# Kernel optimization log

Hardware: AMD Instinct MI355X
Metric: run time of the kernel (lower is better)

## Reference

```python
import jax, jax.numpy as jnp
from jax import lax
import numpy as np

# ---- SLAYER SRM-alpha neuron / simulation constants (net_params) ----
THETA = 10.0      # spiking threshold
TAU_SR = 1.0      # PSP (synaptic response) time constant
TAU_REF = 1.0     # refractory time constant
TS = 1.0          # simulation timestep
POOL_GAIN = 1.1 * THETA  # SLAYER pool layer uses fixed weights = 1.1*theta (sum pool)

# SRM alpha kernel eps[n] = (n*Ts/tau) * exp(1 - n*Ts/tau) = c * n * d^n with
#   d = exp(-Ts/tau), c = e*Ts/tau.  Causal convolution with this kernel obeys
# a 2nd-order linear recurrence, so we implement psp as a lax.scan over time
# (the "recursive exponential temporal filter" the original does via temporal conv).

def psp(x):
    """Alpha-kernel temporal filter along last (time) axis."""
    d = float(np.exp(-TS / TAU_SR))
    c = float(np.e * TS / TAU_SR)
    xt = jnp.moveaxis(x, -1, 0)  # (T, ...)
    z = jnp.zeros_like(xt[0])
    def step(carry, u):
        p, q = carry
        q = d * (q + p)       # q[t] = sum_{n>=1} n d^n x[t-n]
        p = d * p + u         # p[t] = sum_{n>=0} d^n x[t-n]
        return (p, q), c * q
    _, y = lax.scan(step, (z, z), xt)
    return jnp.moveaxis(y, 0, -1)


def spike(u):
    """SLAYER spike generation: threshold the membrane potential at theta and
    subtract a refractory alpha kernel (-2*theta * alpha(tauRef)) from the
    future potential after each spike. Sequential scan over time."""
    d = float(np.exp(-TS / TAU_REF))
    c_r = float(-2.0 * THETA * np.e * TS / TAU_REF)
    ut = jnp.moveaxis(u, -1, 0)  # (T, ...)
    z = jnp.zeros_like(ut[0])
    def step(carry, u_t):
        p, q = carry
        q = d * (q + p)                       # refractory filter state
        s = (u_t + c_r * q >= THETA).astype(u_t.dtype)
        p = d * p + s                         # spikes feed the refractory filter
        return (p, q), s
    _, s = lax.scan(step, (z, z), ut)
    return jnp.moveaxis(s, 0, -1) / TS


def pool(x, k):
    """SLAYER pool: conv with fixed weight 1.1*theta (sum pool scaled)."""
    B, C, H, W, T = x.shape
    xr = x.reshape(B, C, H // k, k, W // k, k, T)
    return POOL_GAIN * xr.sum(axis=(3, 5))


def conv2d_t(x, W, pad):
    """Per-timestep 2D conv (SLAYER conv has time-kernel 1, no bias)."""
    B, C, H, Wd, T = x.shape
    xf = jnp.moveaxis(x, -1, 1).reshape(B * T, C, H, Wd)
    y = lax.conv_general_dilated(xf, W, (1, 1), [(pad, pad), (pad, pad)],
                                 dimension_numbers=('NCHW', 'OIHW', 'NCHW'))
    O, Ho, Wo = y.shape[1], y.shape[2], y.shape[3]
    return jnp.moveaxis(y.reshape(B, T, O, Ho, Wo), 1, -1)


def setup_inputs() -> dict:
    key = jax.random.key(0)
    ks = jax.random.split(key, 5)
    B, T = 8, 300
    s_in = jax.random.bernoulli(ks[0], 0.1, (B, 2, 128, 128, T)).astype(jnp.float32)
    # weightScale 10/50/... only affects init magnitude; choose scales that
    # produce non-degenerate spiking activity.
    W1 = jax.random.normal(ks[1], (16, 2, 5, 5), jnp.float32) * 0.5
    W2 = jax.random.normal(ks[2], (32, 16, 3, 3), jnp.float32) * 0.2
    Wf1 = jax.random.normal(ks[3], (512, 32, 8, 8), jnp.float32) * 0.05
    Wf2 = jax.random.normal(ks[4], (11, 512), jnp.float32) * 0.2
    return {"s_in": s_in, "W1": W1, "W2": W2, "Wf1": Wf1, "Wf2": Wf2}


def reference(s_in, W1, W2, Wf1, Wf2):
    s = spike(psp(pool(s_in, 4)))                 # SP0: (B,2,32,32,T)
    s = spike(psp(conv2d_t(s, W1, 2)))            # SC1: (B,16,32,32,T)
    s = spike(psp(pool(s, 2)))                    # SP1: (B,16,16,16,T)
    # SDC dropout p=0.0 -> identity
    s = spike(psp(conv2d_t(s, W2, 1)))            # SC2: (B,32,16,16,T)
    s = spike(psp(pool(s, 2)))                    # SP2: (B,32,8,8,T)
    # SDF dropout p=0.0 -> identity
    s = spike(psp(jnp.einsum('bchwt,ochw->bot', s, Wf1)))  # SF1: (B,512,T)
    s = spike(psp(jnp.einsum('bct,oc->bot', s, Wf2)))      # SF2: (B,11,T)
    return s
```

## Files before the change

### kernel.cpp

```cpp
#include <hip/hip_runtime.h>
#include <stdint.h>

#define T_STEPS 300
#define T4 75

typedef __attribute__((ext_vector_type(8))) short bf16x8;
typedef __attribute__((ext_vector_type(4))) float f32x4;

__device__ __forceinline__ void scan_step(float x, float& pp, float& pq,
                                          float& rp, float& rq, float& s_out) {
    const float D  = 0.36787944117144233f;
    const float C  = 2.7182818284590452f;
    const float CR = -54.365636569180904f;
    const float TH = 10.0f;
    pq = D * (pq + pp);
    pp = D * pp + x;
    float u = C * pq;
    rq = D * (rq + rp);
    float s = (u + CR * rq >= TH) ? 1.0f : 0.0f;
    rp = D * rp + s;
    s_out = s;
}

#define SCAN4(v, PACK)                                                     \
    {                                                                      \
        float s0, s1, s2, s3;                                              \
        scan_step(v.x, pp, pq, rp, rq, s0);                                \
        scan_step(v.y, pp, pq, rp, rq, s1);                                \
        scan_step(v.z, pp, pq, rp, rq, s2);                                \
        scan_step(v.w, pp, pq, rp, rq, s3);                                \
        PACK = (uint32_t)s0 | ((uint32_t)s1 << 8) |                        \
               ((uint32_t)s2 << 16) | ((uint32_t)s3 << 24);                \
    }

#define FMA4(A, wc) A.x = fmaf(wc, f0, A.x); A.y = fmaf(wc, f1, A.y); \
                    A.z = fmaf(wc, f2, A.z); A.w = fmaf(wc, f3, A.w);

__global__ __launch_bounds__(256) void k_pool4(const float* __restrict__ in,
                                               float* __restrict__ z) {
    int idx = blockIdx.x * 256 + threadIdx.x;
    int t4 = idx % T4;
    int n  = idx / T4;
    int x = n & 31, y = (n >> 5) & 31, bc = n >> 10;
    const float* base = in + ((size_t)bc * 16384 + (size_t)(4 * y) * 128 + 4 * x) * T_STEPS + 4 * t4;
    float4 acc = {0.f, 0.f, 0.f, 0.f};
#pragma unroll
    for (int i = 0; i < 4; ++i)
#pragma unroll
        for (int j = 0; j < 4; ++j) {
            float4 v = *reinterpret_cast<const float4*>(base + ((size_t)i * 128 + j) * T_STEPS);
            acc.x += v.x; acc.y += v.y; acc.z += v.z; acc.w += v.w;
        }
    float4 o = {11.f * acc.x, 11.f * acc.y, 11.f * acc.z, 11.f * acc.w};
    *reinterpret_cast<float4*>(z + (size_t)n * T_STEPS + 4 * t4) = o;
}

__global__ __launch_bounds__(256) void k_scan_l0(const float* __restrict__ z,
                                                 uint32_t* __restrict__ sp, int N) {
    int n = blockIdx.x * 256 + threadIdx.x;
    if (n >= N) return;
    const float4* zp = reinterpret_cast<const float4*>(z + (size_t)n * T_STEPS);
    float pp = 0.f, pq = 0.f, rp = 0.f, rq = 0.f;
#pragma unroll 2
    for (int t4 = 0; t4 < T4; ++t4) {
        float4 v = zp[t4];
        uint32_t pack;
        SCAN4(v, pack);
        sp[(size_t)t4 * N + n] = pack;
    }
}

__global__ __launch_bounds__(256) void k_scan_plane(const float4* __restrict__ z,
                                                    uint32_t* __restrict__ sp, int N) {
    int n = blockIdx.x * 256 + threadIdx.x;
    if (n >= N) return;
    float pp = 0.f, pq = 0.f, rp = 0.f, rq = 0.f;
#pragma unroll 2
    for (int t4 = 0; t4 < T4; ++t4) {
        float4 v = z[(size_t)t4 * N + n];
        uint32_t pack;
        SCAN4(v, pack);
        sp[(size_t)t4 * N + n] = pack;
    }
}

__global__ __launch_bounds__(256) void k_scan_f32(const float* __restrict__ z,
                                                  float* __restrict__ s, int N, int ostride) {
    int n = blockIdx.x * blockDim.x + threadIdx.x;
    if (n >= N) return;
    const float4* zp = reinterpret_cast<const float4*>(z + (size_t)n * T_STEPS);
    float* spo = s + (size_t)n * ostride;
    float pp = 0.f, pq = 0.f, rp = 0.f, rq = 0.f;
    for (int it = 0; it < T4; ++it) {
        float4 v = zp[it];
        float4 o;
        scan_step(v.x, pp, pq, rp, rq, o.x);
        scan_step(v.y, pp, pq, rp, rq, o.y);
        scan_step(v.z, pp, pq, rp, rq, o.z);
        scan_step(v.w, pp, pq, rp, rq, o.w);
        *reinterpret_cast<float4*>(spo + it * 4) = o;
    }
}

template<int HW, int NIN, int NOUT>
__global__ __launch_bounds__(256) void k_pool2s(const uint32_t* __restrict__ sin,
                                                uint32_t* __restrict__ sout) {
    int n = blockIdx.x * 256 + threadIdx.x;
    if (n >= NOUT) return;
    int x = n % HW, y = (n / HW) % HW, bc = n / (HW * HW);
    const int W2d = HW * 2;
    const uint32_t* base0 = sin + (size_t)bc * W2d * W2d + (size_t)(2 * y) * W2d + 2 * x;
    float pp = 0.f, pq = 0.f, rp = 0.f, rq = 0.f;
#pragma unroll 2
    for (int t4 = 0; t4 < T4; ++t4) {
        const uint32_t* p = base0 + (size_t)t4 * NIN;
        uint32_t sum = p[0] + p[1] + p[W2d] + p[W2d + 1];
        float4 v;
        v.x = 11.f * (float)(sum & 0xffu);
        v.y = 11.f * (float)((sum >> 8) & 0xffu);
        v.z = 11.f * (float)((sum >> 16) & 0xffu);
        v.w = 11.f * (float)(sum >> 24);
        uint32_t pack;
        SCAN4(v, pack);
        sout[(size_t)t4 * NOUT + n] = pack;
    }
}

__global__ __launch_bounds__(256) void k_pool2s_bf(const uint32_t* __restrict__ sin,
                                                   ushort* __restrict__ sb) {
    int n = blockIdx.x * 256 + threadIdx.x;
    if (n >= 16384) return;
    int x = n & 7, y = (n >> 3) & 7, bc = n >> 6;
    const uint32_t* base0 = sin + (size_t)bc * 256 + (size_t)(2 * y) * 16 + 2 * x;
    int b = n >> 11, k = n & 2047;
    ushort* out = sb + (size_t)b * 320 * 2048 + k;
    float pp = 0.f, pq = 0.f, rp = 0.f, rq = 0.f;
    for (int t4 = 0; t4 < T4; ++t4) {
        const uint32_t* p = base0 + (size_t)t4 * 65536;
        uint32_t sum = p[0] + p[1] + p[16] + p[17];
        float4 v;
        v.x = 11.f * (float)(sum & 0xffu);
        v.y = 11.f * (float)((sum >> 8) & 0xffu);
        v.z = 11.f * (float)((sum >> 16) & 0xffu);
        v.w = 11.f * (float)(sum >> 24);
        float s0, s1, s2, s3;
        scan_step(v.x, pp, pq, rp, rq, s0);
        scan_step(v.y, pp, pq, rp, rq, s1);
        scan_step(v.z, pp, pq, rp, rq, s2);
        scan_step(v.w, pp, pq, rp, rq, s3);
        out[(size_t)(t4 * 4 + 0) * 2048] = s0 != 0.f ? 0x3F80 : 0;
        out[(size_t)(t4 * 4 + 1) * 2048] = s1 != 0.f ? 0x3F80 : 0;
        out[(size_t)(t4 * 4 + 2) * 2048] = s2 != 0.f ? 0x3F80 : 0;
        out[(size_t)(t4 * 4 + 3) * 2048] = s3 != 0.f ? 0x3F80 : 0;
    }
}

__global__ __launch_bounds__(256) void k_conv1(const uint32_t* __restrict__ s0p,
                                               const float* __restrict__ W1,
                                               float4* __restrict__ z1p) {
    __shared__ float w_lds[2][25][16];
    int bid = blockIdx.x;
    int pixblk = bid & 3;
    int t4 = (bid >> 2) % 75;
    int b  = bid / 300;
    int tid = threadIdx.x;
    for (int j = tid; j < 800; j += 256) {
        int o = j & 15, kk = (j >> 4) % 25, c = j / 400;
        w_lds[c][kk][o] = W1[(o * 2 + c) * 25 + kk];
    }
    __syncthreads();
    int pix = pixblk * 256 + tid;
    int px = pix & 31, py = pix >> 5;
    float4 acc[16];
#pragma unroll
    for (int o = 0; o < 16; ++o) acc[o] = make_float4(0.f, 0.f, 0.f, 0.f);
    const uint32_t* pb = s0p + (size_t)t4 * 16384 + (size_t)(b * 2) * 1024;
    for (int c = 0; c < 2; ++c) {
#pragma unroll
        for (int ky = 0; ky < 5; ++ky) {
            int yy = py + ky - 2;
            bool rok = (unsigned)yy < 32u;
#pragma unroll
            for (int kx = 0; kx < 5; ++kx) {
                int xx = px + kx - 2;
                uint32_t v = 0;
                if (rok && (unsigned)xx < 32u) v = pb[c * 1024 + yy * 32 + xx];
                float f0 = (float)(v & 0xffu), f1 = (float)((v >> 8) & 0xffu);
                float f2 = (float)((v >> 16) & 0xffu), f3 = (float)(v >> 24);
                int kk = ky * 5 + kx;
#pragma unroll
                for (int oo = 0; oo < 4; ++oo) {
                    float4 w4 = *reinterpret_cast<const float4*>(&w_lds[c][kk][oo * 4]);
                    FMA4(acc[oo * 4 + 0], w4.x);
                    FMA4(acc[oo * 4 + 1], w4.y);
                    FMA4(acc[oo * 4 + 2], w4.z);
                    FMA4(acc[oo * 4 + 3], w4.w);
                }
            }
        }
    }
    size_t zb = (size_t)t4 * 131072 + (size_t)(b * 16) * 1024 + pix;
#pragma unroll
    for (int o = 0; o < 16; ++o) z1p[zb + o * 1024] = acc[o];
}

__global__ __launch_bounds__(256) void k_conv2(const uint32_t* __restrict__ s2p,
                                               const float* __restrict__ W2,
                                               float4* __restrict__ z2p) {
    __shared__ float w_lds[16][9][16];
    int bid = blockIdx.x;
    int oh = bid & 1;
    int t4 = (bid >> 1) % 75;
    int b  = bid / 150;
    int tid = threadIdx.x;
    for (int j = tid; j < 2304; j += 256) {
        int o = j & 15;
        int t9 = (j >> 4) % 9;
        int c  = j / 144;
        w_lds[c][t9][o] = W2[(size_t)((oh * 16 + o) * 16 + c) * 9 + t9];
    }
    __syncthreads();
    int px = tid & 15, py = tid >> 4;
    float4 acc[16];
#pragma unroll
    for (int o = 0; o < 16; ++o) acc[o] = make_float4(0.f, 0.f, 0.f, 0.f);
    const uint32_t* pb = s2p + (size_t)t4 * 32768 + (size_t)(b * 16) * 256;
    for (int c = 0; c < 16; ++c) {
#pragma unroll
        for (int ky = 0; ky < 3; ++ky) {
            int yy = py + ky - 1;
            bool rok = (unsigned)yy < 16u;
#pragma unroll
            for (int kx = 0; kx < 3; ++kx) {
                int xx = px + kx - 1;
                uint32_t v = 0;
                if (rok && (unsigned)xx < 16u) v = pb[c * 256 + yy * 16 + xx];
                float f0 = (float)(v & 0xffu), f1 = (float)((v >> 8) & 0xffu);
                float f2 = (float)((v >> 16) & 0xffu), f3 = (float)(v >> 24);
                int t9 = ky * 3 + kx;
#pragma unroll
                for (int oo = 0; oo < 4; ++oo) {
                    float4 w4 = *reinterpret_cast<const float4*>(&w_lds[c][t9][oo * 4]);
                    FMA4(acc[oo * 4 + 0], w4.x);
                    FMA4(acc[oo * 4 + 1], w4.y);
                    FMA4(acc[oo * 4 + 2], w4.z);
                    FMA4(acc[oo * 4 + 3], w4.w);
                }
            }
        }
    }
    size_t zb = (size_t)t4 * 65536 + (size_t)(b * 32 + oh * 16) * 256 + tid;
#pragma unroll
    for (int o = 0; o < 16; ++o) z2p[zb + o * 256] = acc[o];
}

__device__ __forceinline__ ushort f2bf(float f) {
    uint32_t u = __float_as_uint(f);
    u = u + 0x7fffu + ((u >> 16) & 1u);
    return (ushort)(u >> 16);
}
__device__ __forceinline__ float bf2f(ushort h) {
    return __uint_as_float((uint32_t)h << 16);
}
__global__ __launch_bounds__(256) void k_wsplit(const float* __restrict__ W,
                                                ushort* __restrict__ Wh,
                                                ushort* __restrict__ Wm,
                                                ushort* __restrict__ Wl, int n) {
    int i = blockIdx.x * 256 + threadIdx.x;
    if (i >= n) return;
    float w = W[i];
    ushort h = f2bf(w);
    float r1 = w - bf2f(h);
    ushort m = f2bf(r1);
    float r2 = r1 - bf2f(m);
    ushort l = f2bf(r2);
    Wh[i] = h; Wm[i] = m; Wl[i] = l;
}

__device__ __forceinline__ bf16x8 ldb(const ushort* p) {
    return *reinterpret_cast<const bf16x8*>(p);
}
__global__ __launch_bounds__(256) void k_fc1_mfma(const ushort* __restrict__ Wh,
                                                  const ushort* __restrict__ Wm,
                                                  const ushort* __restrict__ Wl,
                                                  const ushort* __restrict__ sb,
                                                  float* __restrict__ z) {
    int bid = blockIdx.x;
    int obk = bid & 7;
    int r   = bid >> 3;
    int tbk = r % 10;
    int b   = r / 10;
    int tid = threadIdx.x, lane = tid & 63, wv = tid >> 6;
    int l15 = lane & 15, l4 = lane >> 4;
    int oA = obk * 64 + (wv & 1) * 32 + l15;
    int t  = tbk * 32 + (wv >> 1) * 16 + l15;
    size_t a0 = (size_t)oA * 2048 + l4 * 8;
    size_t a1 = a0 + 16 * 2048;
    size_t bo = ((size_t)b * 320 + t) * 2048 + l4 * 8;

    f32x4 acc0 = {0.f, 0.f, 0.f, 0.f};
    f32x4 acc1 = {0.f, 0.f, 0.f, 0.f};

    bf16x8 h0 = ldb(Wh + a0), h1 = ldb(Wh + a1);
    bf16x8 m0 = ldb(Wm + a0), m1 = ldb(Wm + a1);
    bf16x8 l0 = ldb(Wl + a0), l1 = ldb(Wl + a1);
    bf16x8 bb = ldb(sb + bo);

    for (int ks = 0; ks < 64; ++ks) {
        int kn = (ks < 63) ? (ks + 1) * 32 : 0;
        bf16x8 nh0 = ldb(Wh + a0 + kn), nh1 = ldb(Wh + a1 + kn);
        bf16x8 nm0 = ldb(Wm + a0 + kn), nm1 = ldb(Wm + a1 + kn);
        bf16x8 nl0 = ldb(Wl + a0 + kn), nl1 = ldb(Wl + a1 + kn);
        bf16x8 nbb = ldb(sb + bo + kn);
        acc0 = __builtin_amdgcn_mfma_f32_16x16x32_bf16(h0, bb, acc0, 0, 0, 0);
        acc1 = __builtin_amdgcn_mfma_f32_16x16x32_bf16(h1, bb, acc1, 0, 0, 0);
        acc0 = __builtin_amdgcn_mfma_f32_16x16x32_bf16(m0, bb, acc0, 0, 0, 0);
        acc1 = __builtin_amdgcn_mfma_f32_16x16x32_bf16(m1, bb, acc1, 0, 0, 0);
        acc0 = __builtin_amdgcn_mfma_f32_16x16x32_bf16(l0, bb, acc0, 0, 0, 0);
        acc1 = __builtin_amdgcn_mfma_f32_16x16x32_bf16(l1, bb, acc1, 0, 0, 0);
        h0 = nh0; h1 = nh1; m0 = nm0; m1 = nm1; l0 = nl0; l1 = nl1; bb = nbb;
    }

    if (t < T_STEPS) {
        int orow = obk * 64 + (wv & 1) * 32 + l4 * 4;
        float* zr = z + ((size_t)b * 512 + orow) * T_STEPS + t;
        zr[0 * T_STEPS] = acc0.x;  zr[1 * T_STEPS] = acc0.y;
        zr[2 * T_STEPS] = acc0.z;  zr[3 * T_STEPS] = acc0.w;
        float* zr2 = zr + 16 * T_STEPS;
        zr2[0 * T_STEPS] = acc1.x; zr2[1 * T_STEPS] = acc1.y;
        zr2[2 * T_STEPS] = acc1.z; zr2[3 * T_STEPS] = acc1.w;
    }
}

__global__ __launch_bounds__(256) void k_fc2(const float* __restrict__ s5,
                                             const float* __restrict__ Wf2,
                                             float* __restrict__ z) {
    int idx = blockIdx.x * 256 + threadIdx.x;
    if (idx >= 6600) return;
    int t4 = idx % T4;
    int r  = idx / T4;
    int b = r & 7, o = r >> 3;
    const float* sp = s5 + (size_t)b * 512 * T_STEPS + 4 * t4;
    const float* wp = Wf2 + (size_t)o * 512;
    float a0 = 0.f, a1 = 0.f, a2 = 0.f, a3 = 0.f;
#pragma unroll 2
    for (int k = 0; k < 512; k += 4) {
        float4 wv = *reinterpret_cast<const float4*>(wp + k);
        float4 v0 = *reinterpret_cast<const float4*>(sp + (size_t)(k + 0) * T_STEPS);
        float4 v1 = *reinterpret_cast<const float4*>(sp + (size_t)(k + 1) * T_STEPS);
        float4 v2 = *reinterpret_cast<const float4*>(sp + (size_t)(k + 2) * T_STEPS);
        float4 v3 = *reinterpret_cast<const float4*>(sp + (size_t)(k + 3) * T_STEPS);
        a0 = fmaf(wv.x, v0.x, a0); a1 = fmaf(wv.x, v0.y, a1); a2 = fmaf(wv.x, v0.z, a2); a3 = fmaf(wv.x, v0.w, a3);
        a0 = fmaf(wv.y, v1.x, a0); a1 = fmaf(wv.y, v1.y, a1); a2 = fmaf(wv.y, v1.z, a2); a3 = fmaf(wv.y, v1.w, a3);
        a0 = fmaf(wv.z, v2.x, a0); a1 = fmaf(wv.z, v2.y, a1); a2 = fmaf(wv.z, v2.z, a2); a3 = fmaf(wv.z, v2.w, a3);
        a0 = fmaf(wv.w, v3.x, a0); a1 = fmaf(wv.w, v3.y, a1); a2 = fmaf(wv.w, v3.z, a2); a3 = fmaf(wv.w, v3.w, a3);
    }
    *reinterpret_cast<float4*>(z + (size_t)(b * 11 + o) * T_STEPS + 4 * t4) = make_float4(a0, a1, a2, a3);
}

__global__ void k_zero(float* out, int n) {
    int i = blockIdx.x * 256 + threadIdx.x;
    if (i < n) out[i] = 0.f;
}

extern "C" void kernel_launch(void* const* d_in, const int* in_sizes, int n_in,
                              void* d_out, int out_size, void* d_ws, size_t ws_size,
                              hipStream_t stream) {
    const float* s_in = (const float*)d_in[0];
    const float* W1   = (const float*)d_in[1];
    const float* W2   = (const float*)d_in[2];
    const float* Wf1  = (const float*)d_in[3];
    const float* Wf2  = (const float*)d_in[4];
    float* out = (float*)d_out;

    const size_t OFF_Z  = 0;
    const size_t OFF_S0 = 157286400;
    const size_t OFF_S1 = 162201600;
    const size_t OFF_S2 = 201523200;
    const size_t OFF_S3 = 211353600;
    const size_t OFF_SB = 231014400;
    const size_t OFF_S5 = 241500160;
    const size_t OFF_WH = 246415360;
    const size_t OFF_WM = 248512512;
    const size_t OFF_WL = 250609664;
    const size_t NEEDED = 252706816;

    if (ws_size < NEEDED) {
        k_zero<<<(26400 + 255) / 256, 256, 0, stream>>>(out, 26400);
        return;
    }

    char* ws = (char*)d_ws;
    float*    Z   = (float*)(ws + OFF_Z);
    uint32_t* s0p = (uint32_t*)(ws + OFF_S0);
    uint32_t* s1p = (uint32_t*)(ws + OFF_S1);
    uint32_t* s2p = (uint32_t*)(ws + OFF_S2);
    uint32_t* s3p = (uint32_t*)(ws + OFF_S3);
    ushort*   sbf = (ushort*)(ws + OFF_SB);
    float*    s5  = (float*)(ws + OFF_S5);
    ushort*   Wh  = (ushort*)(ws + OFF_WH);
    ushort*   Wm  = (ushort*)(ws + OFF_WM);
    ushort*   Wl  = (ushort*)(ws + OFF_WL);

    k_wsplit<<<4096, 256, 0, stream>>>(Wf1, Wh, Wm, Wl, 512 * 2048);

    k_pool4<<<4800, 256, 0, stream>>>(s_in, Z);
    k_scan_l0<<<64, 256, 0, stream>>>(Z, s0p, 16384);

    k_conv1<<<2400, 256, 0, stream>>>(s0p, W1, (float4*)Z);
    k_scan_plane<<<512, 256, 0, stream>>>((const float4*)Z, s1p, 131072);

    k_pool2s<16, 131072, 32768><<<128, 256, 0, stream>>>(s1p, s2p);

    k_conv2<<<1200, 256, 0, stream>>>(s2p, W2, (float4*)Z);
    k_scan_plane<<<256, 256, 0, stream>>>((const float4*)Z, s3p, 65536);

    k_pool2s_bf<<<64, 256, 0, stream>>>(s3p, sbf);

    k_fc1_mfma<<<640, 256, 0, stream>>>(Wh, Wm, Wl, sbf, Z);
    k_scan_f32<<<16, 256, 0, stream>>>(Z, s5, 4096, 300);

    k_fc2<<<26, 256, 0, stream>>>(s5, Wf2, Z);
    k_scan_f32<<<1, 128, 0, stream>>>(Z, out, 88, 300);
}
```

Baseline: 988.5 us.

## Stage FC1 operand tiles in double-buffered LDS for cross-wave reuse

The FC1 MFMA kernel now cooperatively loads 64x32 tiles of the three split-weight planes and the spike operand into double-buffered shared memory. Each wave computes a 2x2 grid of 16x16 MFMA tiles from LDS instead of fetching its own operands from global memory. The block tile grows from 64x32 to 64x64, which halves the grid to 320 blocks. This cuts redundant global and L2 traffic for the weights, at the cost of a barrier per k-step, LDS bank traffic, and fewer blocks in flight.

New measurement: 998.4 us. About the same (+1.0%).

```diff
diff --git a/kernel.cpp b/kernel.cpp
--- a/kernel.cpp
+++ b/kernel.cpp
@@ -277,58 +277,104 @@
     Wh[i] = h; Wm[i] = m; Wl[i] = l;
 }
 
-__device__ __forceinline__ bf16x8 ldb(const ushort* p) {
-    return *reinterpret_cast<const bf16x8*>(p);
-}
 __global__ __launch_bounds__(256) void k_fc1_mfma(const ushort* __restrict__ Wh,
                                                   const ushort* __restrict__ Wm,
                                                   const ushort* __restrict__ Wl,
                                                   const ushort* __restrict__ sb,
                                                   float* __restrict__ z) {
+    __shared__ ushort lds[2][16 * 64 * 8];
+
     int bid = blockIdx.x;
     int obk = bid & 7;
-    int r   = bid >> 3;
-    int tbk = r % 10;
-    int b   = r / 10;
-    int tid = threadIdx.x, lane = tid & 63, wv = tid >> 6;
-    int l15 = lane & 15, l4 = lane >> 4;
-    int oA = obk * 64 + (wv & 1) * 32 + l15;
-    int t  = tbk * 32 + (wv >> 1) * 16 + l15;
-    size_t a0 = (size_t)oA * 2048 + l4 * 8;
-    size_t a1 = a0 + 16 * 2048;
-    size_t bo = ((size_t)b * 320 + t) * 2048 + l4 * 8;
-
-    f32x4 acc0 = {0.f, 0.f, 0.f, 0.f};
-    f32x4 acc1 = {0.f, 0.f, 0.f, 0.f};
-
-    bf16x8 h0 = ldb(Wh + a0), h1 = ldb(Wh + a1);
-    bf16x8 m0 = ldb(Wm + a0), m1 = ldb(Wm + a1);
-    bf16x8 l0 = ldb(Wl + a0), l1 = ldb(Wl + a1);
-    bf16x8 bb = ldb(sb + bo);
-
+    int combo = bid >> 3;
+    int tbk = combo % 5;
+    int b   = combo / 5;
+    int tid = threadIdx.x;
+    int wv = tid >> 6, lane = tid & 63, l15 = lane & 15, l4 = lane >> 4;
+    int o0 = obk * 64, t0 = tbk * 64;
+
+    const ushort* gsrc[4];
+    int ldsoff[4];
+    {
+        const ushort* Wpl[3] = {Wh, Wm, Wl};
+        int r = lane;
+#pragma unroll
+        for (int u = 0; u < 4; ++u) {
+            int s = wv * 4 + u;
+            if (s < 12) {
+                int p = s >> 2, q = s & 3;
+                gsrc[u] = Wpl[p] + (size_t)(o0 + r) * 2048 + q * 8;
+            } else {
+                int q = s - 12;
+                gsrc[u] = sb + ((size_t)b * 320 + t0 + r) * 2048 + q * 8;
+            }
+            ldsoff[u] = (s * 64 + r) * 8;
+        }
+    }
+
+    int rowA = (wv & 1) * 32 + l15;
+    int rowB = (wv >> 1) * 32 + l15;
+    int idxA[3][2], idxB[2];
+#pragma unroll
+    for (int p = 0; p < 3; ++p)
+#pragma unroll
+        for (int i = 0; i < 2; ++i)
+            idxA[p][i] = ((p * 4 + l4) * 64 + rowA + i * 16) * 8;
+#pragma unroll
+    for (int j = 0; j < 2; ++j)
+        idxB[j] = ((12 + l4) * 64 + rowB + j * 16) * 8;
+
+    f32x4 acc00 = {0,0,0,0}, acc01 = {0,0,0,0}, acc10 = {0,0,0,0}, acc11 = {0,0,0,0};
+
+    uint4 rv[4];
+#pragma unroll
+    for (int u = 0; u < 4; ++u)
+        rv[u] = *reinterpret_cast<const uint4*>(gsrc[u]);
+
+    int buf = 0;
     for (int ks = 0; ks < 64; ++ks) {
-        int kn = (ks < 63) ? (ks + 1) * 32 : 0;
-        bf16x8 nh0 = ldb(Wh + a0 + kn), nh1 = ldb(Wh + a1 + kn);
-        bf16x8 nm0 = ldb(Wm + a0 + kn), nm1 = ldb(Wm + a1 + kn);
-        bf16x8 nl0 = ldb(Wl + a0 + kn), nl1 = ldb(Wl + a1 + kn);
-        bf16x8 nbb = ldb(sb + bo + kn);
-        acc0 = __builtin_amdgcn_mfma_f32_16x16x32_bf16(h0, bb, acc0, 0, 0, 0);
-        acc1 = __builtin_amdgcn_mfma_f32_16x16x32_bf16(h1, bb, acc1, 0, 0, 0);
-        acc0 = __builtin_amdgcn_mfma_f32_16x16x32_bf16(m0, bb, acc0, 0, 0, 0);
-        acc1 = __builtin_amdgcn_mfma_f32_16x16x32_bf16(m1, bb, acc1, 0, 0, 0);
-        acc0 = __builtin_amdgcn_mfma_f32_16x16x32_bf16(l0, bb, acc0, 0, 0, 0);
-        acc1 = __builtin_amdgcn_mfma_f32_16x16x32_bf16(l1, bb, acc1, 0, 0, 0);
-        h0 = nh0; h1 = nh1; m0 = nm0; m1 = nm1; l0 = nl0; l1 = nl1; bb = nbb;
-    }
-
-    if (t < T_STEPS) {
-        int orow = obk * 64 + (wv & 1) * 32 + l4 * 4;
-        float* zr = z + ((size_t)b * 512 + orow) * T_STEPS + t;
-        zr[0 * T_STEPS] = acc0.x;  zr[1 * T_STEPS] = acc0.y;
-        zr[2 * T_STEPS] = acc0.z;  zr[3 * T_STEPS] = acc0.w;
-        float* zr2 = zr + 16 * T_STEPS;
-        zr2[0 * T_STEPS] = acc1.x; zr2[1 * T_STEPS] = acc1.y;
-        zr2[2 * T_STEPS] = acc1.z; zr2[3 * T_STEPS] = acc1.w;
+#pragma unroll
+        for (int u = 0; u < 4; ++u)
+            *reinterpret_cast<uint4*>(&lds[buf][ldsoff[u]]) = rv[u];
+        if (ks < 63) {
+            int koff = (ks + 1) * 32;
+#pragma unroll
+            for (int u = 0; u < 4; ++u)
+                rv[u] = *reinterpret_cast<const uint4*>(gsrc[u] + koff);
+        }
+        __syncthreads();
+        bf16x8 B0 = *reinterpret_cast<const bf16x8*>(&lds[buf][idxB[0]]);
+        bf16x8 B1 = *reinterpret_cast<const bf16x8*>(&lds[buf][idxB[1]]);
+#pragma unroll
+        for (int p = 0; p < 3; ++p) {
+            bf16x8 A0 = *reinterpret_cast<const bf16x8*>(&lds[buf][idxA[p][0]]);
+            bf16x8 A1 = *reinterpret_cast<const bf16x8*>(&lds[buf][idxA[p][1]]);
+            acc00 = __builtin_amdgcn_mfma_f32_16x16x32_bf16(A0, B0, acc00, 0, 0, 0);
+            acc01 = __builtin_amdgcn_mfma_f32_16x16x32_bf16(A0, B1, acc01, 0, 0, 0);
+            acc10 = __builtin_amdgcn_mfma_f32_16x16x32_bf16(A1, B0, acc10, 0, 0, 0);
+            acc11 = __builtin_amdgcn_mfma_f32_16x16x32_bf16(A1, B1, acc11, 0, 0, 0);
+        }
+        buf ^= 1;
+    }
+
+    int ob = o0 + (wv & 1) * 32 + l4 * 4;
+    int tb = t0 + (wv >> 1) * 32 + l15;
+#pragma unroll
+    for (int i = 0; i < 2; ++i) {
+        f32x4 ai0 = (i == 0) ? acc00 : acc10;
+        f32x4 ai1 = (i == 0) ? acc01 : acc11;
+#pragma unroll
+        for (int j = 0; j < 2; ++j) {
+            f32x4 a = (j == 0) ? ai0 : ai1;
+            int tcol = tb + j * 16;
+            if (tcol < T_STEPS) {
+                float* zr = z + ((size_t)b * 512 + ob + i * 16) * T_STEPS + tcol;
+                zr[0 * T_STEPS] = a.x;
+                zr[1 * T_STEPS] = a.y;
+                zr[2 * T_STEPS] = a.z;
+                zr[3 * T_STEPS] = a.w;
+            }
+        }
     }
 }
 
@@ -417,7 +463,7 @@
 
     k_pool2s_bf<<<64, 256, 0, stream>>>(s3p, sbf);
 
-    k_fc1_mfma<<<640, 256, 0, stream>>>(Wh, Wm, Wl, sbf, Z);
+    k_fc1_mfma<<<320, 256, 0, stream>>>(Wh, Wm, Wl, sbf, Z);
     k_scan_f32<<<16, 256, 0, stream>>>(Z, s5, 4096, 300);
 
     k_fc2<<<26, 256, 0, stream>>>(s5, Wf2, Z);
```
